# Kernel optimization log

Measured on AMD Instinct MI355X. Metric: run time of the kernel, lower is better.

Reference implementation:

```python
import jax, jax.numpy as jnp
import numpy as np

N = 100000          # number of road-network nodes
E = 640000          # number of directed edges (sparse adjacency nnz)
HID = 128           # hidden_dims = lane(16)+type(32)+length(16)+node(64)
N_LAYERS = 3        # hparams.baseline_gat_layer


def setup_inputs() -> dict:
    key = jax.random.key(0)
    ks = jax.random.split(key, 12)
    inp = {
        'node_feature': jax.random.randint(ks[0], (N,), 0, 100000),
        'type_feature': jax.random.randint(ks[1], (N,), 0, 20),
        'length_feature': jax.random.randint(ks[2], (N,), 0, 100),
        'lane_feature': jax.random.randint(ks[3], (N,), 0, 10),
        'adj_src': jax.random.randint(ks[4], (E,), 0, N),
        'adj_dst': jax.random.randint(ks[5], (E,), 0, N),
        'adj_val': jax.random.uniform(ks[6], (E,), dtype=jnp.float32),
        # learned parameters
        'node_emb': jax.random.normal(ks[7], (100000, 64), dtype=jnp.float32) * 0.02,
        'type_emb': jax.random.normal(ks[8], (20, 32), dtype=jnp.float32) * 0.02,
        'length_emb': jax.random.normal(ks[9], (100, 16), dtype=jnp.float32) * 0.02,
        'lane_emb': jax.random.normal(ks[10], (10, 16), dtype=jnp.float32) * 0.02,
        'W': jax.random.normal(ks[11], (HID, HID), dtype=jnp.float32) / np.sqrt(HID),
        'b': jnp.zeros((HID,), dtype=jnp.float32),
    }
    return inp


def spgcn_layer(x, W, b, adj_src, adj_dst, adj_val):
    # GCN layer: out = spmm(adj, x @ W) + b, adj given as COO edge list
    support = x @ W                                # [N, HID]
    msg = support[adj_src] * adj_val[:, None]      # gather + scale, [E, HID]
    agg = jax.ops.segment_sum(msg, adj_dst, num_segments=N)  # scatter-add
    return agg + b


def reference(node_feature, type_feature, length_feature, lane_feature,
              adj_src, adj_dst, adj_val,
              node_emb, type_emb, length_emb, lane_emb, W, b):
    # embedding lookups + concat: [lane, type, length, node] -> [N, HID]
    raw_feat = jnp.concatenate([
        lane_emb[lane_feature],
        type_emb[type_feature],
        length_emb[length_feature],
        node_emb[node_feature],
    ], axis=1)
    # repeated propagation with the SAME shared SPGCN layer weights
    for _ in range(N_LAYERS):
        raw_feat = spgcn_layer(raw_feat, W, b, adj_src, adj_dst, adj_val)
    return raw_feat
```

## Files before the change

### kernel.cpp

```cpp
#include <hip/hip_runtime.h>
#include <hip/hip_bf16.h>

typedef __hip_bfloat16 bf16;
typedef unsigned short ushort_t;
typedef __attribute__((ext_vector_type(8))) short short8;
typedef __attribute__((ext_vector_type(4))) float f32x4;

#define NN 100000
#define NE 640000
#define HD 128
#define NB 391
#define EMB_U 6250
#define PREP_U 64
#define CNT_U 391
#define HIST_U 2500
#define GEMM_U 782
#define AGG_U 6250
#define D_U 391
#define LDA 136


__device__ __forceinline__ float bf2f(ushort_t u) {
    unsigned v = (unsigned)u << 16;
    return __builtin_bit_cast(float, v);
}
__device__ __forceinline__ ushort_t f2bf(float f) {
    bf16 h = __float2bfloat16(f);
    return *(ushort_t*)&h;
}

struct P {
    const int *nodef, *typef, *lenf, *lanef, *adj_src, *adj_dst;
    const float *adj_val, *node_emb, *type_emb, *len_emb, *lane_emb, *W, *bias;
    ushort_t *Xa, *Xb, *Wt, *w2t, *w3t;
    float *bw, *bw2, *d, *d2;
    int *cnt, *offs, *slots, *bsum;
    int2 *epack;
    float *outf;
};


__global__ __launch_bounds__(256) void prep_k(P p) {
    const int v = blockIdx.x;
    const int tid = threadIdx.x;
    if (v < CNT_U) {
        const int idx = v * 256 + tid;
        if (idx < NN) p.cnt[idx] = 0;
    } else {
        const int idx = (v - CNT_U) * 256 + tid;
        const int n = idx >> 7, k = idx & 127;
        p.Wt[idx] = f2bf(p.W[(size_t)k * HD + n]);
    }
}

__global__ __launch_bounds__(256) void ehist_k(P p) {
    const int tid = threadIdx.x;
    if (blockIdx.x >= 1 + HIST_U) {
        const int idx = (blockIdx.x - 1 - HIST_U) * 256 + tid;
        const int i = idx >> 4;
        const int c = (idx & 15) * 8;
        const float* tbl; size_t base;
        if (c < 16)      { tbl = p.lane_emb; base = (size_t)p.lanef[i] * 16 + c; }
        else if (c < 48) { tbl = p.type_emb; base = (size_t)p.typef[i] * 32 + (c - 16); }
        else if (c < 64) { tbl = p.len_emb;  base = (size_t)p.lenf[i]  * 16 + (c - 48); }
        else             { tbl = p.node_emb; base = (size_t)p.nodef[i] * 64 + (c - 64); }
        const float4 f0 = *(const float4*)(tbl + base);
        const float4 f1 = *(const float4*)(tbl + base + 4);
        ushort_t u8[8] = { f2bf(f0.x), f2bf(f0.y), f2bf(f0.z), f2bf(f0.w),
                           f2bf(f1.x), f2bf(f1.y), f2bf(f1.z), f2bf(f1.w) };
        *(uint4*)(p.Xa + (size_t)i * HD + c) = *(uint4*)u8;
        return;
    }
    if (blockIdx.x >= 1) {
        const int e = (blockIdx.x - 1) * 256 + tid;
        p.slots[e] = atomicAdd(&p.cnt[p.adj_dst[e]], 1);
        return;
    }
    __shared__ ushort_t WtL[HD * HD];
    __shared__ float bwS[HD];
    for (int i = tid; i < HD * HD / 8; i += 256)
        *(uint4*)&WtL[i * 8] = *(const uint4*)&p.Wt[i * 8];
    __syncthreads();

    const int w = tid >> 6;
    const int ln = tid & 15;
    const int quad = (tid >> 4) & 3;
    const int koff = quad * 8;
    const f32x4 zero = {0.f, 0.f, 0.f, 0.f};

    short8 bfrg[2][4];
#pragma unroll
    for (int nt = 0; nt < 2; ++nt)
#pragma unroll
        for (int kc = 0; kc < 4; ++kc)
            bfrg[nt][kc] = *(const short8*)&WtL[(w * 32 + nt * 16 + ln) * HD + kc * 32 + koff];

#pragma unroll
    for (int mt = 0; mt < 8; ++mt) {
        const int m = mt * 16 + ln;
        short8 afrg[4];
#pragma unroll
        for (int kc = 0; kc < 4; ++kc) {
            ushort_t a[8];
#pragma unroll
            for (int j = 0; j < 8; ++j)
                a[j] = WtL[(kc * 32 + koff + j) * HD + m];
            afrg[kc] = *(short8*)a;
        }
        f32x4 acc[2] = {zero, zero};
#pragma unroll
        for (int nt = 0; nt < 2; ++nt)
#pragma unroll
            for (int kc = 0; kc < 4; ++kc)
                acc[nt] = __builtin_amdgcn_mfma_f32_16x16x32_bf16(
                        afrg[kc], bfrg[nt][kc], acc[nt], 0, 0, 0);
#pragma unroll
        for (int nt = 0; nt < 2; ++nt)
#pragma unroll
            for (int reg = 0; reg < 4; ++reg) {
                const int col = w * 32 + nt * 16 + ln;
                const int row = mt * 16 + quad * 4 + reg;
                p.w2t[col * HD + row] = f2bf(acc[nt][reg]);
            }
    }
    __syncthreads();

#pragma unroll
    for (int mt = 0; mt < 8; ++mt) {
        const int m = mt * 16 + ln;
        short8 afrg[4];
#pragma unroll
        for (int kc = 0; kc < 4; ++kc) {
            ushort_t a[8];
#pragma unroll
            for (int j = 0; j < 8; ++j)
                a[j] = p.w2t[(kc * 32 + koff + j) * HD + m];
            afrg[kc] = *(short8*)a;
        }
        f32x4 acc[2] = {zero, zero};
#pragma unroll
        for (int nt = 0; nt < 2; ++nt)
#pragma unroll
            for (int kc = 0; kc < 4; ++kc)
                acc[nt] = __builtin_amdgcn_mfma_f32_16x16x32_bf16(
                        afrg[kc], bfrg[nt][kc], acc[nt], 0, 0, 0);
#pragma unroll
        for (int nt = 0; nt < 2; ++nt)
#pragma unroll
            for (int reg = 0; reg < 4; ++reg) {
                const int col = w * 32 + nt * 16 + ln;
                const int row = mt * 16 + quad * 4 + reg;
                p.w3t[col * HD + row] = f2bf(acc[nt][reg]);
            }
    }
    __syncthreads();

    if (tid < HD) {
        float s = 0.f;
        for (int k = 0; k < HD; ++k) s += p.bias[k] * bf2f(WtL[tid * HD + k]);
        bwS[tid] = s;
        p.bw[tid] = s;
    }
    __syncthreads();
    if (tid < HD) {
        float s = 0.f;
        for (int k = 0; k < HD; ++k) s += bwS[k] * bf2f(WtL[tid * HD + k]);
        p.bw2[tid] = s;
    }
}


__global__ __launch_bounds__(256) void scan1_k(P p) {
    __shared__ int s[256];
    const int tid = threadIdx.x;
    const int idx = blockIdx.x * 256 + tid;
    s[tid] = (idx < NN) ? p.cnt[idx] : 0;
    __syncthreads();
    for (int o = 128; o; o >>= 1) {
        if (tid < o) s[tid] += s[tid + o];
        __syncthreads();
    }
    if (tid == 0) p.bsum[blockIdx.x] = s[0];
}

__global__ __launch_bounds__(256) void scan3_k(P p) {
    __shared__ int s[256];
    const int b = blockIdx.x;
    const int tid = threadIdx.x;
    int acc = 0;
    for (int i = tid; i < b; i += 256) acc += p.bsum[i];
    s[tid] = acc;
    __syncthreads();
    for (int o = 128; o; o >>= 1) {
        if (tid < o) s[tid] += s[tid + o];
        __syncthreads();
    }
    const int boffv = s[0];
    __syncthreads();
    const int idx = b * 256 + tid;
    int v = (idx < NN) ? p.cnt[idx] : 0;
    s[tid] = v;
    __syncthreads();
    for (int o = 1; o < 256; o <<= 1) {
        int x = (tid >= o) ? s[tid - o] : 0;
        __syncthreads();
        s[tid] += x;
        __syncthreads();
    }
    const int excl = s[tid] - v + boffv;
    if (idx <= NN) p.offs[idx] = excl;
}

__global__ __launch_bounds__(256) void pos_k(P p) {
    const int e = blockIdx.x * 256 + threadIdx.x;
    const int dst = p.adj_dst[e];
    int2 pk;
    pk.x = p.adj_src[e];
    pk.y = __float_as_int(p.adj_val[e]);
    p.epack[p.offs[dst] + p.slots[e]] = pk;
}

__global__ __launch_bounds__(256) void agg_k(P p, const ushort_t* __restrict__ Xin,
                                             ushort_t* __restrict__ Xout, int aux) {
    if (blockIdx.x >= AGG_U) {
        const int node = (blockIdx.x - AGG_U) * 256 + threadIdx.x;
        if (node < NN) {
            const int lo = p.offs[node], hi = p.offs[node + 1];
            float s = 0.f;
            if (aux == 1) {
                for (int j = lo; j < hi; ++j) s += __int_as_float(p.epack[j].y);
                p.d[node] = s;
            } else {
                for (int j = lo; j < hi; ++j) {
                    const int2 e = p.epack[j];
                    s += __int_as_float(e.y) * p.d[e.x];
                }
                p.d2[node] = s;
            }
        }
        return;
    }
    const int node = blockIdx.x * 16 + (threadIdx.x >> 4);
    const int lane = threadIdx.x & 15;
    const int c = lane * 8;
    const int lo = p.offs[node];
    const int hi = p.offs[node + 1];
    float a0[8], a1[8], a2[8], a3[8];
#pragma unroll
    for (int k = 0; k < 8; ++k) { a0[k] = a1[k] = a2[k] = a3[k] = 0.f; }
    int j = lo;
    for (; j + 3 < hi; j += 4) {
        const int2 e0 = p.epack[j], e1 = p.epack[j + 1];
        const int2 e2 = p.epack[j + 2], e3 = p.epack[j + 3];
        const short8 u0 = *(const short8*)(Xin + (size_t)e0.x * HD + c);
        const short8 u1 = *(const short8*)(Xin + (size_t)e1.x * HD + c);
        const short8 u2 = *(const short8*)(Xin + (size_t)e2.x * HD + c);
        const short8 u3 = *(const short8*)(Xin + (size_t)e3.x * HD + c);
        const float v0 = __int_as_float(e0.y), v1 = __int_as_float(e1.y);
        const float v2 = __int_as_float(e2.y), v3 = __int_as_float(e3.y);
#pragma unroll
        for (int k = 0; k < 8; ++k) {
            a0[k] += bf2f((ushort_t)u0[k]) * v0;
            a1[k] += bf2f((ushort_t)u1[k]) * v1;
            a2[k] += bf2f((ushort_t)u2[k]) * v2;
            a3[k] += bf2f((ushort_t)u3[k]) * v3;
        }
    }
    for (; j < hi; ++j) {
        const int2 e0 = p.epack[j];
        const float v0 = __int_as_float(e0.y);
        const short8 u0 = *(const short8*)(Xin + (size_t)e0.x * HD + c);
#pragma unroll
        for (int k = 0; k < 8; ++k) a0[k] += bf2f((ushort_t)u0[k]) * v0;
    }
    ushort_t u8[8];
#pragma unroll
    for (int k = 0; k < 8; ++k) u8[k] = f2bf((a0[k] + a1[k]) + (a2[k] + a3[k]));
    *(uint4*)(Xout + (size_t)node * HD + c) = *(uint4*)u8;
}

__global__ __launch_bounds__(256) void gemmf_k(P p, const ushort_t* __restrict__ X2) {
    __shared__ ushort_t Xs[128 * LDA];
    const int tid = threadIdx.x;
    const int row0 = blockIdx.x * 128;

    {
        const int g = tid >> 4;
        const int lane = tid & 15;
        const int c = lane * 8;
        for (int mi = 0; mi < 8; ++mi) {
            const int m = g * 8 + mi;
            const int gm = row0 + m;
            float a0[8], a1[8], a2[8], a3[8];
#pragma unroll
            for (int k = 0; k < 8; ++k) { a0[k] = a1[k] = a2[k] = a3[k] = 0.f; }
            if (gm < NN) {
                const int lo = p.offs[gm];
                const int hi = p.offs[gm + 1];
                int j = lo;
                for (; j + 3 < hi; j += 4) {
                    const int2 e0 = p.epack[j], e1 = p.epack[j + 1];
                    const int2 e2 = p.epack[j + 2], e3 = p.epack[j + 3];
                    const short8 u0 = *(const short8*)(X2 + (size_t)e0.x * HD + c);
                    const short8 u1 = *(const short8*)(X2 + (size_t)e1.x * HD + c);
                    const short8 u2 = *(const short8*)(X2 + (size_t)e2.x * HD + c);
                    const short8 u3 = *(const short8*)(X2 + (size_t)e3.x * HD + c);
                    const float v0 = __int_as_float(e0.y), v1 = __int_as_float(e1.y);
                    const float v2 = __int_as_float(e2.y), v3 = __int_as_float(e3.y);
#pragma unroll
                    for (int k = 0; k < 8; ++k) {
                        a0[k] += bf2f((ushort_t)u0[k]) * v0;
                        a1[k] += bf2f((ushort_t)u1[k]) * v1;
                        a2[k] += bf2f((ushort_t)u2[k]) * v2;
                        a3[k] += bf2f((ushort_t)u3[k]) * v3;
                    }
                }
                for (; j < hi; ++j) {
                    const int2 e0 = p.epack[j];
                    const float v0 = __int_as_float(e0.y);
                    const short8 u0 = *(const short8*)(X2 + (size_t)e0.x * HD + c);
#pragma unroll
                    for (int k = 0; k < 8; ++k) a0[k] += bf2f((ushort_t)u0[k]) * v0;
                }
            }
            ushort_t u8[8];
#pragma unroll
            for (int k = 0; k < 8; ++k) u8[k] = f2bf((a0[k] + a1[k]) + (a2[k] + a3[k]));
            *(uint4*)&Xs[m * LDA + c] = *(uint4*)u8;
        }
    }

    const int w = tid >> 6;
    const int ln = tid & 15;
    const int quad = (tid >> 4) & 3;
    const int koff = quad * 8;
    const int col0 = w * 32 + ln;
    const int col1 = col0 + 16;

    short8 bfrg[2][4];
#pragma unroll
    for (int nt = 0; nt < 2; ++nt)
#pragma unroll
        for (int kc = 0; kc < 4; ++kc)
            bfrg[nt][kc] = *(const short8*)&p.w3t[(size_t)(w * 32 + nt * 16 + ln) * HD + kc * 32 + koff];

    const float bwc0 = p.bw[col0],  bwc1 = p.bw[col1];
    const float bw2c0 = p.bw2[col0], bw2c1 = p.bw2[col1];
    const float bc0 = p.bias[col0], bc1 = p.bias[col1];

    __syncthreads();

    const f32x4 zero = {0.f, 0.f, 0.f, 0.f};
#pragma unroll
    for (int mt = 0; mt < 8; ++mt) {
        short8 afrg[4];
#pragma unroll
        for (int kc = 0; kc < 4; ++kc)
            afrg[kc] = *(const short8*)&Xs[(mt * 16 + ln) * LDA + kc * 32 + koff];
        f32x4 acc[2] = {zero, zero};
#pragma unroll
        for (int nt = 0; nt < 2; ++nt)
#pragma unroll
            for (int kc = 0; kc < 4; ++kc)
                acc[nt] = __builtin_amdgcn_mfma_f32_16x16x32_bf16(
                        afrg[kc], bfrg[nt][kc], acc[nt], 0, 0, 0);
#pragma unroll
        for (int reg = 0; reg < 4; ++reg) {
            const int gm = row0 + mt * 16 + quad * 4 + reg;
            if (gm < NN) {
                const float dg = p.d[gm], d2g = p.d2[gm];
                p.outf[(size_t)gm * HD + col0] = acc[0][reg] + d2g * bw2c0 + dg * bwc0 + bc0;
                p.outf[(size_t)gm * HD + col1] = acc[1][reg] + d2g * bw2c1 + dg * bwc1 + bc1;
            }
        }
    }
}

extern "C" void kernel_launch(void* const* d_in, const int* in_sizes, int n_in,
                              void* d_out, int out_size, void* d_ws, size_t ws_size,
                              hipStream_t stream) {
    P p;
    p.nodef    = (const int*)d_in[0];
    p.typef    = (const int*)d_in[1];
    p.lenf     = (const int*)d_in[2];
    p.lanef    = (const int*)d_in[3];
    p.adj_src  = (const int*)d_in[4];
    p.adj_dst  = (const int*)d_in[5];
    p.adj_val  = (const float*)d_in[6];
    p.node_emb = (const float*)d_in[7];
    p.type_emb = (const float*)d_in[8];
    p.len_emb  = (const float*)d_in[9];
    p.lane_emb = (const float*)d_in[10];
    p.W        = (const float*)d_in[11];
    p.bias     = (const float*)d_in[12];
    p.outf     = (float*)d_out;

    const size_t xbytes = (size_t)NN * HD * 2;
    char* wp = (char*)d_ws;
    p.Xa    = (ushort_t*)wp; wp += xbytes;
    p.Xb    = (ushort_t*)wp; wp += xbytes;
    p.cnt   = (int*)wp;      wp += (size_t)NN * 4;
    p.offs  = (int*)wp;      wp += 400016;
    p.slots = (int*)wp;      wp += (size_t)NE * 4;
    p.epack = (int2*)wp;     wp += (size_t)NE * 8;
    p.Wt    = (ushort_t*)wp; wp += 32768;
    p.w2t   = (ushort_t*)wp; wp += 32768;
    p.w3t   = (ushort_t*)wp; wp += 32768;
    p.bw    = (float*)wp;    wp += 512;
    p.bw2   = (float*)wp;    wp += 512;
    p.d     = (float*)wp;    wp += (size_t)NN * 4;
    p.d2    = (float*)wp;    wp += (size_t)NN * 4;
    p.bsum  = (int*)wp;      wp += 1600;

    prep_k<<<CNT_U + PREP_U, 256, 0, stream>>>(p);
    ehist_k<<<1 + HIST_U + EMB_U, 256, 0, stream>>>(p);
    scan1_k<<<NB, 256, 0, stream>>>(p);
    scan3_k<<<NB, 256, 0, stream>>>(p);
    pos_k<<<HIST_U, 256, 0, stream>>>(p);
    agg_k<<<AGG_U + D_U, 256, 0, stream>>>(p, p.Xa, p.Xb, 1);
    agg_k<<<AGG_U + D_U, 256, 0, stream>>>(p, p.Xb, p.Xa, 2);
    gemmf_k<<<GEMM_U, 256, 0, stream>>>(p, p.Xa);
}
```

Baseline: 292.6 us.

## Drop prep kernel, read W directly in weight-power block, halve final GEMM tile

Removes the prep kernel that zeroed counters and built a transposed bf16 W. The counters are now cleared with a memset, and the weight-power block in ehist_k reads the fp32 W directly and converts it to bf16 in registers, so no LDS staging of W is needed. The final fused aggregate+GEMM kernel now processes 64 rows per block instead of 128, doubling the block count to improve occupancy and load balance. The trade-offs are more uncoalesced global reads of W in the single serial weight block, and weight fragments reloaded by twice as many GEMM blocks.

```diff
diff --git a/kernel.cpp b/kernel.cpp
--- a/kernel.cpp
+++ b/kernel.cpp
@@ -11,10 +11,8 @@
 #define HD 128
 #define NB 391
 #define EMB_U 6250
-#define PREP_U 64
-#define CNT_U 391
 #define HIST_U 2500
-#define GEMM_U 782
+#define GEMM_U 1563
 #define AGG_U 6250
 #define D_U 391
 #define LDA 136
@@ -32,28 +30,15 @@
 struct P {
     const int *nodef, *typef, *lenf, *lanef, *adj_src, *adj_dst;
     const float *adj_val, *node_emb, *type_emb, *len_emb, *lane_emb, *W, *bias;
-    ushort_t *Xa, *Xb, *Wt, *w2t, *w3t;
+    ushort_t *Xa, *Xb, *w2t, *w3t;
     float *bw, *bw2, *d, *d2;
     int *cnt, *offs, *slots, *bsum;
     int2 *epack;
     float *outf;
 };
 
-
-__global__ __launch_bounds__(256) void prep_k(P p) {
-    const int v = blockIdx.x;
-    const int tid = threadIdx.x;
-    if (v < CNT_U) {
-        const int idx = v * 256 + tid;
-        if (idx < NN) p.cnt[idx] = 0;
-    } else {
-        const int idx = (v - CNT_U) * 256 + tid;
-        const int n = idx >> 7, k = idx & 127;
-        p.Wt[idx] = f2bf(p.W[(size_t)k * HD + n]);
-    }
-}
-
 __global__ __launch_bounds__(256) void ehist_k(P p) {
+    __shared__ float bwS[HD];
     const int tid = threadIdx.x;
     if (blockIdx.x >= 1 + HIST_U) {
         const int idx = (blockIdx.x - 1 - HIST_U) * 256 + tid;
@@ -76,12 +61,6 @@
         p.slots[e] = atomicAdd(&p.cnt[p.adj_dst[e]], 1);
         return;
     }
-    __shared__ ushort_t WtL[HD * HD];
-    __shared__ float bwS[HD];
-    for (int i = tid; i < HD * HD / 8; i += 256)
-        *(uint4*)&WtL[i * 8] = *(const uint4*)&p.Wt[i * 8];
-    __syncthreads();
-
     const int w = tid >> 6;
     const int ln = tid & 15;
     const int quad = (tid >> 4) & 3;
@@ -92,8 +71,13 @@
 #pragma unroll
     for (int nt = 0; nt < 2; ++nt)
 #pragma unroll
-        for (int kc = 0; kc < 4; ++kc)
-            bfrg[nt][kc] = *(const short8*)&WtL[(w * 32 + nt * 16 + ln) * HD + kc * 32 + koff];
+        for (int kc = 0; kc < 4; ++kc) {
+            ushort_t b8[8];
+#pragma unroll
+            for (int j = 0; j < 8; ++j)
+                b8[j] = f2bf(p.W[(size_t)(kc * 32 + koff + j) * HD + w * 32 + nt * 16 + ln]);
+            bfrg[nt][kc] = *(short8*)b8;
+        }
 
 #pragma unroll
     for (int mt = 0; mt < 8; ++mt) {
@@ -101,11 +85,11 @@
         short8 afrg[4];
 #pragma unroll
         for (int kc = 0; kc < 4; ++kc) {
-            ushort_t a[8];
-#pragma unroll
-            for (int j = 0; j < 8; ++j)
-                a[j] = WtL[(kc * 32 + koff + j) * HD + m];
-            afrg[kc] = *(short8*)a;
+            const float4 f0 = *(const float4*)&p.W[(size_t)m * HD + kc * 32 + koff];
+            const float4 f1 = *(const float4*)&p.W[(size_t)m * HD + kc * 32 + koff + 4];
+            ushort_t a8[8] = { f2bf(f0.x), f2bf(f0.y), f2bf(f0.z), f2bf(f0.w),
+                               f2bf(f1.x), f2bf(f1.y), f2bf(f1.z), f2bf(f1.w) };
+            afrg[kc] = *(short8*)a8;
         }
         f32x4 acc[2] = {zero, zero};
 #pragma unroll
@@ -153,18 +137,17 @@
                 p.w3t[col * HD + row] = f2bf(acc[nt][reg]);
             }
     }
-    __syncthreads();
 
     if (tid < HD) {
         float s = 0.f;
-        for (int k = 0; k < HD; ++k) s += p.bias[k] * bf2f(WtL[tid * HD + k]);
+        for (int k = 0; k < HD; ++k) s += p.bias[k] * p.W[(size_t)k * HD + tid];
         bwS[tid] = s;
         p.bw[tid] = s;
     }
     __syncthreads();
     if (tid < HD) {
         float s = 0.f;
-        for (int k = 0; k < HD; ++k) s += bwS[k] * bf2f(WtL[tid * HD + k]);
+        for (int k = 0; k < HD; ++k) s += bwS[k] * p.W[(size_t)k * HD + tid];
         p.bw2[tid] = s;
     }
 }
@@ -280,16 +263,17 @@
 }
 
 __global__ __launch_bounds__(256) void gemmf_k(P p, const ushort_t* __restrict__ X2) {
-    __shared__ ushort_t Xs[128 * LDA];
+    __shared__ ushort_t Xs[64 * LDA];
     const int tid = threadIdx.x;
-    const int row0 = blockIdx.x * 128;
+    const int row0 = blockIdx.x * 64;
 
     {
         const int g = tid >> 4;
         const int lane = tid & 15;
         const int c = lane * 8;
-        for (int mi = 0; mi < 8; ++mi) {
-            const int m = g * 8 + mi;
+#pragma unroll
+        for (int mi = 0; mi < 4; ++mi) {
+            const int m = g * 4 + mi;
             const int gm = row0 + m;
             float a0[8], a1[8], a2[8], a3[8];
 #pragma unroll
@@ -352,7 +336,7 @@
 
     const f32x4 zero = {0.f, 0.f, 0.f, 0.f};
 #pragma unroll
-    for (int mt = 0; mt < 8; ++mt) {
+    for (int mt = 0; mt < 4; ++mt) {
         short8 afrg[4];
 #pragma unroll
         for (int kc = 0; kc < 4; ++kc)
@@ -403,7 +387,6 @@
     p.offs  = (int*)wp;      wp += 400016;
     p.slots = (int*)wp;      wp += (size_t)NE * 4;
     p.epack = (int2*)wp;     wp += (size_t)NE * 8;
-    p.Wt    = (ushort_t*)wp; wp += 32768;
     p.w2t   = (ushort_t*)wp; wp += 32768;
     p.w3t   = (ushort_t*)wp; wp += 32768;
     p.bw    = (float*)wp;    wp += 512;
@@ -412,7 +395,7 @@
     p.d2    = (float*)wp;    wp += (size_t)NN * 4;
     p.bsum  = (int*)wp;      wp += 1600;
 
-    prep_k<<<CNT_U + PREP_U, 256, 0, stream>>>(p);
+    hipMemsetAsync(p.cnt, 0, (size_t)NN * 4, stream);
     ehist_k<<<1 + HIST_U + EMB_U, 256, 0, stream>>>(p);
     scan1_k<<<NB, 256, 0, stream>>>(p);
     scan3_k<<<NB, 256, 0, stream>>>(p);
```

New measurement: 296.3 us. Within noise of the previous version (+1.3%).
